# Optimization experiments

Hardware: AMD Instinct MI355X
Metric: run time of the kernel (lower is better)

Reference implementation:

```python
import jax, jax.numpy as jnp
import numpy as np

E = 8          # num_experts
R = 16         # lora rank
TOP_K = 2
SCALING = 32.0 / 16.0   # lora_alpha / r
D_IN = 4096
D_OUT = 4096


def setup_inputs() -> dict:
    key = jax.random.key(0)
    ks = jax.random.split(key, 6)
    x = jax.random.normal(ks[0], (4, 2048, D_IN), jnp.float32)
    Wb = jax.random.normal(ks[1], (D_OUT, D_IN), jnp.float32) * 0.02
    bias = jax.random.normal(ks[2], (D_OUT,), jnp.float32) * 0.02
    Wr = jax.random.normal(ks[3], (E, D_IN), jnp.float32) * 0.01  # router (normal init, std=0.01)
    A = jax.random.normal(ks[4], (E, R, D_IN), jnp.float32) * (1.0 / np.sqrt(D_IN))  # kaiming-ish
    Bm = jax.random.normal(ks[5], (E, D_OUT, R), jnp.float32) * 0.01  # nonzero for nontrivial baseline
    return {"x": x, "Wb": Wb, "bias": bias, "Wr": Wr, "A": A, "Bm": Bm}


def reference(x, Wb, bias, Wr, A, Bm):
    # x: [B, S, D_IN]
    xf = x.reshape(-1, x.shape[-1])                       # [T, D_IN]
    T = xf.shape[0]

    # Router: softmax -> top-k -> renormalize selected probs
    logits = xf @ Wr.T                                    # [T, E]
    probs = jax.nn.softmax(logits, axis=-1)
    topk_p, topk_i = jax.lax.top_k(probs, TOP_K)          # [T, K]
    topk_p = topk_p / jnp.sum(topk_p, axis=-1, keepdims=True)

    # Dense per-token expert weights via scatter-add (equivalent to masked dispatch/combine)
    w = jnp.zeros((T, E), xf.dtype).at[jnp.arange(T)[:, None], topk_i].add(topk_p)  # [T, E]

    # LoRA: x @ A_e^T @ B_e^T, weighted combine (dropout = identity, p=0)
    h = jnp.einsum('ti,eri->ter', xf, A)                  # [T, E, R] (small: rank-16)
    lora = jnp.einsum('ter,te,eor->to', h, w, Bm) * SCALING  # [T, D_OUT]

    base = xf @ Wb.T + bias                               # [T, D_OUT]
    out = (base + lora).reshape(*x.shape[:-1], D_OUT)
    return out
```

## Files before the change

kernel.cpp:

```cpp
#include <hip/hip_runtime.h>
#include <cmath>

typedef unsigned short ushort_t;
typedef __attribute__((ext_vector_type(8))) short short8;
typedef __attribute__((ext_vector_type(4))) float f32x4;

#define D_IN   4096
#define D_OUT  4096
#define T_TOK  8192
#define E_EXP  8
#define R_RANK 16
#define KCAT   4224
#define SCALE_LORA 2.0f

__device__ __forceinline__ ushort_t f2bf(float f) {
    unsigned int u = __float_as_uint(f);
    u += 0x7fffu + ((u >> 16) & 1u);
    return (ushort_t)(u >> 16);
}

__global__ __launch_bounds__(256) void build_weights(
    const float* __restrict__ Wb, const float* __restrict__ Bm,
    const float* __restrict__ A, ushort_t* __restrict__ Wcat,
    ushort_t* __restrict__ Abf) {
    int b = blockIdx.x;
    int tid = threadIdx.x;
    if (b < D_OUT) {
        const float4* src = (const float4*)(Wb + (size_t)b * D_IN);
        ushort_t* drow = Wcat + (size_t)b * KCAT;
        for (int c4 = tid; c4 < D_IN / 4; c4 += 256) {
            float4 v = src[c4];
            ushort4 o;
            o.x = f2bf(v.x); o.y = f2bf(v.y); o.z = f2bf(v.z); o.w = f2bf(v.w);
            ((ushort4*)drow)[c4] = o;
        }
        if (tid < E_EXP * R_RANK) {
            int e = tid >> 4, r = tid & 15;
            drow[D_IN + tid] = f2bf(Bm[((size_t)e * D_OUT + b) * R_RANK + r]);
        }
    } else {
        int er = b - D_OUT;
        const float4* src = (const float4*)(A + (size_t)er * D_IN);
        ushort_t* drow = Abf + (size_t)er * D_IN;
        for (int c4 = tid; c4 < D_IN / 4; c4 += 256) {
            float4 v = src[c4];
            ushort4 o;
            o.x = f2bf(v.x); o.y = f2bf(v.y); o.z = f2bf(v.z); o.w = f2bf(v.w);
            ((ushort4*)drow)[c4] = o;
        }
    }
}

__global__ __launch_bounds__(256) void router_convert(
    const float* __restrict__ x, const float* __restrict__ Wr,
    ushort_t* __restrict__ xcat, int2* __restrict__ eids,
    float2* __restrict__ wts) {
    __shared__ float sWr[4 * D_IN];
    int tid = threadIdx.x;
    int lane = tid & 63;
    int wave = tid >> 6;
    int tbase = blockIdx.x * 16 + wave * 4;

    float acc[4][E_EXP];
#pragma unroll
    for (int tk = 0; tk < 4; tk++)
#pragma unroll
        for (int e = 0; e < E_EXP; e++) acc[tk][e] = 0.f;

#pragma unroll
    for (int half = 0; half < 2; half++) {
        __syncthreads();
        {
            const float4* wsrc = (const float4*)(Wr + (size_t)half * 4 * D_IN);
            float4* wdst = (float4*)sWr;
#pragma unroll
            for (int q = 0; q < 16; q++)
                wdst[tid + q * 256] = wsrc[tid + q * 256];
        }
        __syncthreads();

        for (int c4 = lane; c4 < D_IN / 4; c4 += 64) {
            float4 wv[4];
#pragma unroll
            for (int e4 = 0; e4 < 4; e4++)
                wv[e4] = ((const float4*)(sWr + (size_t)e4 * D_IN))[c4];
#pragma unroll
            for (int tk = 0; tk < 4; tk++) {
                int t = tbase + tk;
                float4 v = ((const float4*)(x + (size_t)t * D_IN))[c4];
                if (half == 0) {
                    ushort4 o;
                    o.x = f2bf(v.x); o.y = f2bf(v.y); o.z = f2bf(v.z); o.w = f2bf(v.w);
                    ((ushort4*)(xcat + (size_t)t * KCAT))[c4] = o;
                }
#pragma unroll
                for (int e4 = 0; e4 < 4; e4++)
                    acc[tk][half * 4 + e4] +=
                        v.x * wv[e4].x + v.y * wv[e4].y + v.z * wv[e4].z + v.w * wv[e4].w;
            }
        }
    }

#pragma unroll
    for (int tk = 0; tk < 4; tk++)
#pragma unroll
        for (int e = 0; e < E_EXP; e++) {
#pragma unroll
            for (int off = 32; off > 0; off >>= 1)
                acc[tk][e] += __shfl_xor(acc[tk][e], off, 64);
        }
    if (lane == 0) {
#pragma unroll
        for (int tk = 0; tk < 4; tk++) {
            int t = tbase + tk;
            int e0 = 0; float l0 = acc[tk][0];
#pragma unroll
            for (int e = 1; e < E_EXP; e++)
                if (acc[tk][e] > l0) { l0 = acc[tk][e]; e0 = e; }
            int e1 = -1; float l1 = -3.4e38f;
#pragma unroll
            for (int e = 0; e < E_EXP; e++)
                if (e != e0 && acc[tk][e] > l1) { l1 = acc[tk][e]; e1 = e; }
            float w0 = 1.f / (1.f + expf(l1 - l0));
            eids[t] = make_int2(e0, e1);
            wts[t] = make_float2(w0, 1.f - w0);
        }
    }
}

__global__ __launch_bounds__(256) void h_gemm_v(
    const ushort_t* __restrict__ Abf, const int2* __restrict__ eids,
    const float2* __restrict__ wts, ushort_t* __restrict__ xcat) {
    __shared__ __align__(16) ushort_t lA[32 * 64];
    __shared__ __align__(16) ushort_t lB[128 * 64];
    int tid = threadIdx.x;
    int lane = tid & 63, wave = tid >> 6;
    int rowBase = blockIdx.x * 32;
    const ushort_t* gA = xcat + (size_t)rowBase * KCAT;

    int rA = tid >> 3;
    int kk = (tid & 7) * 8;
    ushort_t* dA = lA + (size_t)wave * 512;

    f32x4 acc[2][2];
#pragma unroll
    for (int i = 0; i < 2; i++)
#pragma unroll
        for (int j = 0; j < 2; j++)
            acc[i][j] = (f32x4){0.f, 0.f, 0.f, 0.f};

    int n0 = wave * 32;
    int row16 = lane & 15, q8 = (lane >> 4) * 8;

    for (int kt = 0; kt < D_IN; kt += 64) {
        __syncthreads();
        __builtin_amdgcn_global_load_lds(
            (const __attribute__((address_space(1))) unsigned int*)(gA + (size_t)rA * KCAT + kt + kk),
            (__attribute__((address_space(3))) unsigned int*)dA, 16, 0, 0);
#pragma unroll
        for (int q = 0; q < 4; q++) {
            __builtin_amdgcn_global_load_lds(
                (const __attribute__((address_space(1))) unsigned int*)(
                    Abf + (size_t)((tid >> 3) + 32 * q) * D_IN + kt + kk),
                (__attribute__((address_space(3))) unsigned int*)(
                    lB + (size_t)q * 2048 + (size_t)wave * 512), 16, 0, 0);
        }
        __syncthreads();

        short8 af[2][2], bfrag[2][2];
#pragma unroll
        for (int i = 0; i < 2; i++)
#pragma unroll
            for (int kc = 0; kc < 2; kc++)
                af[i][kc] = *(const short8*)&lA[(i * 16 + row16) * 64 + kc * 32 + q8];
#pragma unroll
        for (int j = 0; j < 2; j++)
#pragma unroll
            for (int kc = 0; kc < 2; kc++)
                bfrag[j][kc] = *(const short8*)&lB[(n0 + j * 16 + row16) * 64 + kc * 32 + q8];
#pragma unroll
        for (int i = 0; i < 2; i++)
#pragma unroll
            for (int j = 0; j < 2; j++) {
                acc[i][j] = __builtin_amdgcn_mfma_f32_16x16x32_bf16(
                    af[i][0], bfrag[j][0], acc[i][j], 0, 0, 0);
                acc[i][j] = __builtin_amdgcn_mfma_f32_16x16x32_bf16(
                    af[i][1], bfrag[j][1], acc[i][j], 0, 0, 0);
            }
    }

#pragma unroll
    for (int i = 0; i < 2; i++) {
        int rbase = rowBase + i * 16 + (lane >> 4) * 4;
#pragma unroll
        for (int reg = 0; reg < 4; reg++) {
            int t = rbase + reg;
            int2 e = eids[t];
            float2 w = wts[t];
#pragma unroll
            for (int j = 0; j < 2; j++) {
                int c = n0 + j * 16 + (lane & 15);
                int ce = c >> 4;
                float coef = (ce == e.x) ? (SCALE_LORA * w.x)
                           : ((ce == e.y) ? (SCALE_LORA * w.y) : 0.f);
                xcat[(size_t)t * KCAT + D_IN + c] = f2bf(coef * acc[i][j][reg]);
            }
        }
    }
}

#define NKT 66
#define NIT 33

__global__ __launch_bounds__(512, 2) void gemm_bt_main(
    const ushort_t* __restrict__ Am, const ushort_t* __restrict__ Bmat,
    float* __restrict__ C, const float* __restrict__ bias) {
    __shared__ __align__(16) ushort_t lds[2][2][2][128][64];
    const int lda = KCAT, ldb = KCAT, ldc = D_OUT;
    int tid = threadIdx.x;
    int lane = tid & 63, wave = tid >> 6;
    int wm = wave >> 2, wn = wave & 3;

    int id = ((blockIdx.x & 7) << 6) | (blockIdx.x >> 3);
    int band = id >> 6, wi = id & 63;
    int mt = ((band >> 1) << 3) | (wi & 7);
    int nt = ((band & 1) << 3) | (wi >> 3);
    const int rowBase = mt * 256, colBase = nt * 256;

    const ushort_t* gA = Am + (size_t)rowBase * lda;
    const ushort_t* gB = Bmat + (size_t)colBase * ldb;

    const int srow = tid >> 3;
    const int scol = (((tid & 7) ^ (srow & 7)) << 3);

#define STAGE(MAT, SRC, LD, BUF, KT)                                           \
    {                                                                          \
        _Pragma("unroll")                                                      \
        for (int h = 0; h < 2; h++) {                                          \
            _Pragma("unroll")                                                  \
            for (int q = 0; q < 2; q++) {                                      \
                __builtin_amdgcn_global_load_lds(                              \
                    (const __attribute__((address_space(1))) unsigned int*)(   \
                        (SRC) + (size_t)(h * 128 + q * 64 + srow) * (LD) +     \
                        (KT) + scol),                                          \
                    (__attribute__((address_space(3))) unsigned int*)(         \
                        &lds[BUF][MAT][h][0][0] + q * 4096 + wave * 512),      \
                    16, 0, 0);                                                 \
            }                                                                  \
        }                                                                      \
    }

    int cSwz[2];
#pragma unroll
    for (int kc = 0; kc < 2; kc++)
        cSwz[kc] = (kc * 64 + (lane >> 4) * 16) ^ ((lane & 7) << 4);
    const int rOff = (lane & 15) * 128;
    const int bRow = (wn & 1) * 64 * 128;

    const char* baseA = (const char*)&lds[0][0][wm][0][0];
    const char* baseB = (const char*)&lds[0][1][wn >> 1][0][0];

    f32x4 acc[8][4];
#pragma unroll
    for (int i = 0; i < 8; i++)
#pragma unroll
        for (int j = 0; j < 4; j++) acc[i][j] = (f32x4){0.f, 0.f, 0.f, 0.f};

    short8 aF[4][2], bF[2][2];

#define READ_A(BUF, S)                                                         \
    _Pragma("unroll")                                                          \
    for (int m4 = 0; m4 < 4; m4++) {                                           \
        _Pragma("unroll")                                                      \
        for (int kc = 0; kc < 2; kc++)                                         \
            aF[m4][kc] = *(const short8*)(baseA + (BUF) * 65536 +              \
                ((S) * 4 + m4) * 2048 + rOff + cSwz[kc]);                      \
    }

#define READ_B(BUF, U)                                                         \
    _Pragma("unroll")                                                          \
    for (int n2 = 0; n2 < 2; n2++) {                                           \
        _Pragma("unroll")                                                      \
        for (int kc = 0; kc < 2; kc++)                                         \
            bF[n2][kc] = *(const short8*)(baseB + (BUF) * 65536 + bRow +       \
                ((U) * 2 + n2) * 2048 + rOff + cSwz[kc]);                      \
    }

#define MFMA16(S, U)                                                           \
    __builtin_amdgcn_s_setprio(1);                                             \
    _Pragma("unroll")                                                          \
    for (int m4 = 0; m4 < 4; m4++) {                                           \
        _Pragma("unroll")                                                      \
        for (int n2 = 0; n2 < 2; n2++) {                                       \
            _Pragma("unroll")                                                  \
            for (int kc = 0; kc < 2; kc++)                                     \
                acc[(S) * 4 + m4][(U) * 2 + n2] =                              \
                    __builtin_amdgcn_mfma_f32_16x16x32_bf16(                   \
                        aF[m4][kc], bF[n2][kc],                                \
                        acc[(S) * 4 + m4][(U) * 2 + n2], 0, 0, 0);             \
        }                                                                      \
    }                                                                          \
    __builtin_amdgcn_s_setprio(0);

#define MIDBAR()                                                               \
    __builtin_amdgcn_s_barrier();                                              \
    asm volatile("s_waitcnt lgkmcnt(0)" ::: "memory");

#define ENDBAR() __builtin_amdgcn_s_barrier();

    STAGE(0, gA, lda, 0, 0)
    STAGE(1, gB, ldb, 0, 0)
    STAGE(0, gA, lda, 1, 64)
    asm volatile("s_waitcnt vmcnt(4)" ::: "memory");
    __builtin_amdgcn_s_barrier();

    for (int it = 0; it < NIT; ++it) {
        int ktB1 = (2 * it + 1) * 64;
        int t2 = 2 * it + 2; if (t2 > NKT - 1) t2 = NKT - 1;
        int t3 = 2 * it + 3; if (t3 > NKT - 1) t3 = NKT - 1;
        int kt2 = t2 * 64, kt3 = t3 * 64;

        READ_A(0, 0) READ_B(0, 0)
        STAGE(1, gB, ldb, 1, ktB1)
        MIDBAR() MFMA16(0, 0) ENDBAR()

        READ_B(0, 1)
        MIDBAR() MFMA16(0, 1) ENDBAR()

        READ_A(0, 1)
        MIDBAR() MFMA16(1, 1) ENDBAR()

        READ_B(0, 0)
        STAGE(0, gA, lda, 0, kt2)
        MIDBAR() MFMA16(1, 0)
        asm volatile("s_waitcnt vmcnt(4)" ::: "memory");
        ENDBAR()

        READ_A(1, 0) READ_B(1, 0)
        STAGE(1, gB, ldb, 0, kt2)
        MIDBAR() MFMA16(0, 0) ENDBAR()

        READ_B(1, 1)
        MIDBAR() MFMA16(0, 1) ENDBAR()

        READ_A(1, 1)
        MIDBAR() MFMA16(1, 1) ENDBAR()

        READ_B(1, 0)
        STAGE(0, gA, lda, 1, kt3)
        MIDBAR() MFMA16(1, 0)
        asm volatile("s_waitcnt vmcnt(4)" ::: "memory");
        ENDBAR()
    }

    int r0 = rowBase + wm * 128 + (lane >> 4) * 4;
    int c0 = colBase + wn * 64 + (lane & 15);
#pragma unroll
    for (int mf = 0; mf < 8; mf++) {
#pragma unroll
        for (int nf = 0; nf < 4; nf++) {
            int cc = c0 + nf * 16;
            float badd = bias[cc];
#pragma unroll
            for (int reg = 0; reg < 4; reg++)
                C[(size_t)(r0 + mf * 16 + reg) * ldc + cc] = acc[mf][nf][reg] + badd;
        }
    }
}

extern "C" void kernel_launch(void* const* d_in, const int* in_sizes, int n_in,
                              void* d_out, int out_size, void* d_ws, size_t ws_size,
                              hipStream_t stream) {
    const float* x    = (const float*)d_in[0];
    const float* Wb   = (const float*)d_in[1];
    const float* bias = (const float*)d_in[2];
    const float* Wr   = (const float*)d_in[3];
    const float* A    = (const float*)d_in[4];
    const float* Bm   = (const float*)d_in[5];
    float* out = (float*)d_out;

    char* p = (char*)d_ws;
    ushort_t* xcat = (ushort_t*)p; p += (size_t)T_TOK * KCAT * 2;
    ushort_t* Wcat = (ushort_t*)p; p += (size_t)D_OUT * KCAT * 2;
    ushort_t* Abf  = (ushort_t*)p; p += (size_t)(E_EXP * R_RANK) * D_IN * 2;
    int2*     eids = (int2*)p;     p += (size_t)T_TOK * sizeof(int2);
    float2*   wts  = (float2*)p;   p += (size_t)T_TOK * sizeof(float2);

    build_weights<<<D_OUT + E_EXP * R_RANK, 256, 0, stream>>>(Wb, Bm, A, Wcat, Abf);
    router_convert<<<T_TOK / 16, 256, 0, stream>>>(x, Wr, xcat, eids, wts);
    h_gemm_v<<<T_TOK / 32, 256, 0, stream>>>(Abf, eids, wts, xcat);
    gemm_bt_main<<<(T_TOK / 256) * (D_OUT / 256), 512, 0, stream>>>(xcat, Wcat, out, bias);
}
```

Baseline: 585.7 us.

## Triple-buffer h_gemm LDS staging with XOR swizzle; single-pass router over all experts

The LoRA down-projection kernel moves from a single LDS buffer with two barriers per k-step to a three-stage ring of async global-to-LDS loads, using vmcnt waits so loads overlap MFMA work. It also adds an XOR swizzle on the LDS columns to reduce bank conflicts, and raises wave priority around the MFMAs. The router kernel now loads all 8 expert rows of Wr into shared memory at once, so x is read in a single pass instead of two. The trade is more LDS per block (128KB for the router, triple buffers for h_gemm), which can lower occupancy.

```diff
diff --git a/kernel.cpp b/kernel.cpp
--- a/kernel.cpp
+++ b/kernel.cpp
@@ -55,49 +55,43 @@
     const float* __restrict__ x, const float* __restrict__ Wr,
     ushort_t* __restrict__ xcat, int2* __restrict__ eids,
     float2* __restrict__ wts) {
-    __shared__ float sWr[4 * D_IN];
+    __shared__ float sWr[E_EXP * D_IN];
     int tid = threadIdx.x;
     int lane = tid & 63;
     int wave = tid >> 6;
     int tbase = blockIdx.x * 16 + wave * 4;
 
+    {
+        const float4* wsrc = (const float4*)Wr;
+        float4* wdst = (float4*)sWr;
+#pragma unroll
+        for (int q = 0; q < 32; q++)
+            wdst[tid + q * 256] = wsrc[tid + q * 256];
+    }
+    __syncthreads();
+
     float acc[4][E_EXP];
 #pragma unroll
     for (int tk = 0; tk < 4; tk++)
 #pragma unroll
         for (int e = 0; e < E_EXP; e++) acc[tk][e] = 0.f;
 
-#pragma unroll
-    for (int half = 0; half < 2; half++) {
-        __syncthreads();
-        {
-            const float4* wsrc = (const float4*)(Wr + (size_t)half * 4 * D_IN);
-            float4* wdst = (float4*)sWr;
-#pragma unroll
-            for (int q = 0; q < 16; q++)
-                wdst[tid + q * 256] = wsrc[tid + q * 256];
-        }
-        __syncthreads();
-
-        for (int c4 = lane; c4 < D_IN / 4; c4 += 64) {
-            float4 wv[4];
-#pragma unroll
-            for (int e4 = 0; e4 < 4; e4++)
-                wv[e4] = ((const float4*)(sWr + (size_t)e4 * D_IN))[c4];
-#pragma unroll
-            for (int tk = 0; tk < 4; tk++) {
-                int t = tbase + tk;
-                float4 v = ((const float4*)(x + (size_t)t * D_IN))[c4];
-                if (half == 0) {
-                    ushort4 o;
-                    o.x = f2bf(v.x); o.y = f2bf(v.y); o.z = f2bf(v.z); o.w = f2bf(v.w);
-                    ((ushort4*)(xcat + (size_t)t * KCAT))[c4] = o;
-                }
-#pragma unroll
-                for (int e4 = 0; e4 < 4; e4++)
-                    acc[tk][half * 4 + e4] +=
-                        v.x * wv[e4].x + v.y * wv[e4].y + v.z * wv[e4].z + v.w * wv[e4].w;
-            }
+    for (int c4 = lane; c4 < D_IN / 4; c4 += 64) {
+        float4 wv[E_EXP];
+#pragma unroll
+        for (int e = 0; e < E_EXP; e++)
+            wv[e] = ((const float4*)(sWr + (size_t)e * D_IN))[c4];
+#pragma unroll
+        for (int tk = 0; tk < 4; tk++) {
+            int t = tbase + tk;
+            float4 v = ((const float4*)(x + (size_t)t * D_IN))[c4];
+            ushort4 o;
+            o.x = f2bf(v.x); o.y = f2bf(v.y); o.z = f2bf(v.z); o.w = f2bf(v.w);
+            ((ushort4*)(xcat + (size_t)t * KCAT))[c4] = o;
+#pragma unroll
+            for (int e = 0; e < E_EXP; e++)
+                acc[tk][e] +=
+                    v.x * wv[e].x + v.y * wv[e].y + v.z * wv[e].z + v.w * wv[e].w;
         }
     }
 
@@ -131,16 +125,32 @@
 __global__ __launch_bounds__(256) void h_gemm_v(
     const ushort_t* __restrict__ Abf, const int2* __restrict__ eids,
     const float2* __restrict__ wts, ushort_t* __restrict__ xcat) {
-    __shared__ __align__(16) ushort_t lA[32 * 64];
-    __shared__ __align__(16) ushort_t lB[128 * 64];
+    __shared__ __align__(16) ushort_t lA[3][32 * 64];
+    __shared__ __align__(16) ushort_t lB[3][128 * 64];
     int tid = threadIdx.x;
     int lane = tid & 63, wave = tid >> 6;
     int rowBase = blockIdx.x * 32;
     const ushort_t* gA = xcat + (size_t)rowBase * KCAT;
 
-    int rA = tid >> 3;
-    int kk = (tid & 7) * 8;
-    ushort_t* dA = lA + (size_t)wave * 512;
+    const int srow = tid >> 3;
+    const int scol = (((tid & 7) ^ (srow & 7)) << 3);
+
+#define HSTAGE(BUF, KT)                                                        \
+    {                                                                          \
+        __builtin_amdgcn_global_load_lds(                                      \
+            (const __attribute__((address_space(1))) unsigned int*)(           \
+                gA + (size_t)srow * KCAT + (KT) + scol),                       \
+            (__attribute__((address_space(3))) unsigned int*)(                 \
+                &lA[BUF][0] + wave * 512), 16, 0, 0);                          \
+        _Pragma("unroll")                                                      \
+        for (int q = 0; q < 4; q++) {                                          \
+            __builtin_amdgcn_global_load_lds(                                  \
+                (const __attribute__((address_space(1))) unsigned int*)(       \
+                    Abf + (size_t)(srow + 32 * q) * D_IN + (KT) + scol),       \
+                (__attribute__((address_space(3))) unsigned int*)(             \
+                    &lB[BUF][0] + q * 2048 + wave * 512), 16, 0, 0);           \
+        }                                                                      \
+    }
 
     f32x4 acc[2][2];
 #pragma unroll
@@ -150,43 +160,50 @@
             acc[i][j] = (f32x4){0.f, 0.f, 0.f, 0.f};
 
     int n0 = wave * 32;
-    int row16 = lane & 15, q8 = (lane >> 4) * 8;
-
-    for (int kt = 0; kt < D_IN; kt += 64) {
-        __syncthreads();
-        __builtin_amdgcn_global_load_lds(
-            (const __attribute__((address_space(1))) unsigned int*)(gA + (size_t)rA * KCAT + kt + kk),
-            (__attribute__((address_space(3))) unsigned int*)dA, 16, 0, 0);
-#pragma unroll
-        for (int q = 0; q < 4; q++) {
-            __builtin_amdgcn_global_load_lds(
-                (const __attribute__((address_space(1))) unsigned int*)(
-                    Abf + (size_t)((tid >> 3) + 32 * q) * D_IN + kt + kk),
-                (__attribute__((address_space(3))) unsigned int*)(
-                    lB + (size_t)q * 2048 + (size_t)wave * 512), 16, 0, 0);
-        }
-        __syncthreads();
-
-        short8 af[2][2], bfrag[2][2];
+    int row16 = lane & 15;
+    int cSwz[2];
+#pragma unroll
+    for (int kc = 0; kc < 2; kc++)
+        cSwz[kc] = (kc * 64 + (lane >> 4) * 16) ^ ((row16 & 7) << 4);
+
+    HSTAGE(0, 0)
+    HSTAGE(1, 64)
+    asm volatile("s_waitcnt vmcnt(5)" ::: "memory");
+    __builtin_amdgcn_s_barrier();
+
+    for (int t = 0; t < 64; ++t) {
+        int cur = t % 3;
+        int tn = (t + 2 < 64) ? (t + 2) : 63;
+        HSTAGE((t + 2) % 3, tn * 64)
+        asm volatile("s_waitcnt vmcnt(10)" ::: "memory");
+        __builtin_amdgcn_s_barrier();
+
+        short8 af[2][2], bfr[2][2];
 #pragma unroll
         for (int i = 0; i < 2; i++)
 #pragma unroll
             for (int kc = 0; kc < 2; kc++)
-                af[i][kc] = *(const short8*)&lA[(i * 16 + row16) * 64 + kc * 32 + q8];
+                af[i][kc] = *(const short8*)((const char*)&lA[cur][0] +
+                    (i * 16 + row16) * 128 + cSwz[kc]);
 #pragma unroll
         for (int j = 0; j < 2; j++)
 #pragma unroll
             for (int kc = 0; kc < 2; kc++)
-                bfrag[j][kc] = *(const short8*)&lB[(n0 + j * 16 + row16) * 64 + kc * 32 + q8];
+                bfr[j][kc] = *(const short8*)((const char*)&lB[cur][0] +
+                    (n0 + j * 16 + row16) * 128 + cSwz[kc]);
+
+        __builtin_amdgcn_s_setprio(1);
 #pragma unroll
         for (int i = 0; i < 2; i++)
 #pragma unroll
             for (int j = 0; j < 2; j++) {
                 acc[i][j] = __builtin_amdgcn_mfma_f32_16x16x32_bf16(
-                    af[i][0], bfrag[j][0], acc[i][j], 0, 0, 0);
+                    af[i][0], bfr[j][0], acc[i][j], 0, 0, 0);
                 acc[i][j] = __builtin_amdgcn_mfma_f32_16x16x32_bf16(
-                    af[i][1], bfrag[j][1], acc[i][j], 0, 0, 0);
+                    af[i][1], bfr[j][1], acc[i][j], 0, 0, 0);
             }
+        __builtin_amdgcn_s_setprio(0);
+        __builtin_amdgcn_s_barrier();
     }
 
 #pragma unroll
@@ -207,6 +224,7 @@
             }
         }
     }
+#undef HSTAGE
 }
 
 #define NKT 66
```

New measurement: 559.8 us. 1.05x faster.
